# Kernel tuning notes

Hardware: AMD Instinct MI355X
Metric: run time of the kernel (lower is better)

## Reference

```python
import jax, jax.numpy as jnp
import numpy as np

DIM = 1024
NUM_HEADS = 16
REL_DIM = 32
B, N = 8, 512


def setup_inputs() -> dict:
    key = jax.random.key(0)
    ks = jax.random.split(key, 8)
    s = 0.02
    return {
        "x": jax.random.normal(ks[0], (B, N, DIM), dtype=jnp.float32),
        "rel_bias": jax.random.normal(ks[1], (B, N, N, REL_DIM), dtype=jnp.float32),
        # torch nn.Linear convention: weight (out_features, in_features)
        "W_qkv": jax.random.normal(ks[2], (3 * DIM, DIM), dtype=jnp.float32) * s,
        "b_qkv": jax.random.normal(ks[3], (3 * DIM,), dtype=jnp.float32) * s,
        "W_rel": jax.random.normal(ks[4], (NUM_HEADS, REL_DIM), dtype=jnp.float32) * s,
        "b_rel": jax.random.normal(ks[5], (NUM_HEADS,), dtype=jnp.float32) * s,
        "W_out": jax.random.normal(ks[6], (DIM, DIM), dtype=jnp.float32) * s,
        "b_out": jax.random.normal(ks[7], (DIM,), dtype=jnp.float32) * s,
    }


def reference(x, rel_bias, W_qkv, b_qkv, W_rel, b_rel, W_out, b_out):
    Bx, Nx, D = x.shape
    H = NUM_HEADS
    hd = D // H
    # QKV projection: (B,N,3D) -> (B,N,3,H,hd)
    qkv = (x @ W_qkv.T + b_qkv).reshape(Bx, Nx, 3, H, hd)
    q, k, v = qkv[:, :, 0], qkv[:, :, 1], qkv[:, :, 2]
    scale = hd ** -0.5
    attn = jnp.einsum('bnhd,bmhd->bhnm', q, k) * scale
    # per-pair relative bias projected to heads: (B,N,N,H) -> (B,H,N,N)
    rel = (rel_bias @ W_rel.T + b_rel).transpose(0, 3, 1, 2)
    attn = jax.nn.softmax(attn + rel, axis=-1)
    out = jnp.einsum('bhnm,bmhd->bnhd', attn, v).reshape(Bx, Nx, D)
    return out @ W_out.T + b_out
```

## Files before the change

kernel.cpp:

```cpp
#include <hip/hip_runtime.h>

typedef unsigned short u16;
typedef unsigned int u32;
typedef __attribute__((ext_vector_type(8))) __bf16 bf16x8;
typedef __attribute__((ext_vector_type(4))) float f32x4;

union U8 {
  bf16x8 b;
  uint2 u2[2];
  uint4 u4;
  u16 us[8];
};

__device__ __forceinline__ u16 f2bf(float f) {
  u32 x = __float_as_uint(f);
  x += 0x7FFFu + ((x >> 16) & 1u);
  return (u16)(x >> 16);
}
__device__ __forceinline__ float bf2f(u16 u) {
  return __uint_as_float(((u32)u) << 16);
}

#define GLOAD16(gp, lp)                                                          \
  __builtin_amdgcn_global_load_lds(                                              \
      (const __attribute__((address_space(1))) unsigned int*)(const void*)(gp),  \
      (__attribute__((address_space(3))) unsigned int*)(void*)(lp), 16, 0, 0)

__global__ void k_convert(const float* __restrict__ src, u16* __restrict__ dst, int n4) {
  int idx = blockIdx.x * blockDim.x + threadIdx.x;
  int stride = gridDim.x * blockDim.x;
  for (int i = idx; i < n4; i += stride) {
    float4 v = ((const float4*)src)[i];
    ushort4 o;
    o.x = f2bf(v.x); o.y = f2bf(v.y); o.z = f2bf(v.z); o.w = f2bf(v.w);
    ((ushort4*)dst)[i] = o;
  }
}

__global__ __launch_bounds__(256) void k_rel(const float* __restrict__ rb,
                                             const float* __restrict__ Wr,
                                             const float* __restrict__ br,
                                             u16* __restrict__ out) {
  __shared__ float Wl[16][32];
  __shared__ float bl[16];
  int t = threadIdx.x;
  ((float*)Wl)[t] = Wr[t];
  ((float*)Wl)[t + 256] = Wr[t + 256];
  if (t < 16) bl[t] = br[t];
  __syncthreads();

  size_t row = (size_t)blockIdx.x * 256 + t;
  int m = (int)(row & 511);
  int n = (int)((row >> 9) & 511);
  int b = (int)(row >> 18);
  const float4* rp = (const float4*)(rb + row * 32);
  float4 r4[8];
#pragma unroll
  for (int j = 0; j < 8; ++j) r4[j] = rp[j];

  size_t obase = (size_t)b * 4194304 + (size_t)n * 512 + m;
#pragma unroll
  for (int h = 0; h < 16; ++h) {
    float acc = bl[h];
    const float* w = Wl[h];
#pragma unroll
    for (int j = 0; j < 8; ++j) {
      acc += r4[j].x * w[4 * j + 0] + r4[j].y * w[4 * j + 1] +
             r4[j].z * w[4 * j + 2] + r4[j].w * w[4 * j + 3];
    }
    out[obase + (size_t)h * 262144] = f2bf(acc);
  }
}

template <int MODE>
__global__ __launch_bounds__(256) void k_gemm(const u16* __restrict__ A,
                                              const u16* __restrict__ Bm,
                                              const float* __restrict__ bias,
                                              u16* __restrict__ Qo, u16* __restrict__ Ko,
                                              u16* __restrict__ Vo, float* __restrict__ Co,
                                              int K) {
  __shared__ u16 Al[128 * 64];
  __shared__ u16 Bl[128 * 64];
  const int t = threadIdx.x;
  const int lane = t & 63, wid = t >> 6;
  const int g = lane >> 4, i16 = lane & 15;
  const int wm = wid >> 1, wn = wid & 1;
  const int bm = blockIdx.y, bn = blockIdx.x;

  f32x4 zero = {0.f, 0.f, 0.f, 0.f};
  f32x4 acc[4][4];
#pragma unroll
  for (int mi = 0; mi < 4; ++mi)
#pragma unroll
    for (int ni = 0; ni < 4; ++ni) acc[mi][ni] = zero;

  int srow[4], sgc[4];
#pragma unroll
  for (int i = 0; i < 4; ++i) {
    int ch = wid * 256 + i * 64 + lane;
    int r = ch >> 3, cs = ch & 7;
    srow[i] = r;
    sgc[i] = cs ^ (r & 7);
  }

  for (int k0 = 0; k0 < K; k0 += 64) {
    __syncthreads();
#pragma unroll
    for (int i = 0; i < 4; ++i) {
      const u16* ga = A + (size_t)(bm * 128 + srow[i]) * K + k0 + sgc[i] * 8;
      const u16* gb = Bm + (size_t)(bn * 128 + srow[i]) * K + k0 + sgc[i] * 8;
      u16* la = Al + (size_t)(wid * 256 + i * 64) * 8;
      u16* lb = Bl + (size_t)(wid * 256 + i * 64) * 8;
      GLOAD16(ga, la);
      GLOAD16(gb, lb);
    }
    __syncthreads();

#pragma unroll
    for (int kk = 0; kk < 2; ++kk) {
      U8 af[4], bfr[4];
#pragma unroll
      for (int mi = 0; mi < 4; ++mi) {
        int row = wm * 64 + mi * 16 + i16;
        int ch = (g + 4 * kk) ^ (row & 7);
        af[mi].u4 = *(const uint4*)(Al + row * 64 + ch * 8);
      }
#pragma unroll
      for (int ni = 0; ni < 4; ++ni) {
        int row = wn * 64 + ni * 16 + i16;
        int ch = (g + 4 * kk) ^ (row & 7);
        bfr[ni].u4 = *(const uint4*)(Bl + row * 64 + ch * 8);
      }
#pragma unroll
      for (int mi = 0; mi < 4; ++mi)
#pragma unroll
        for (int ni = 0; ni < 4; ++ni)
          acc[mi][ni] = __builtin_amdgcn_mfma_f32_16x16x32_bf16(af[mi].b, bfr[ni].b,
                                                                acc[mi][ni], 0, 0, 0);
    }
  }

#pragma unroll
  for (int mi = 0; mi < 4; ++mi) {
#pragma unroll
    for (int ni = 0; ni < 4; ++ni) {
      int colb = bn * 128 + wn * 64 + ni * 16;
      int col = colb + i16;
#pragma unroll
      for (int j = 0; j < 4; ++j) {
        int row = bm * 128 + wm * 64 + mi * 16 + 4 * g + j;
        float v = acc[mi][ni][j] + bias[col];
        if (MODE == 0) {
          int tt = col >> 10;
          int h = (col >> 6) & 15;
          int d = col & 63;
          int b = row >> 9;
          int n = row & 511;
          u16* dst = (tt == 0) ? Qo : ((tt == 1) ? Ko : Vo);
          dst[((size_t)(b * 16 + h) * 512 + n) * 64 + d] = f2bf(v);
        } else {
          Co[(size_t)row * 1024 + col] = v;
        }
      }
    }
  }
}

__global__ __launch_bounds__(256) void k_vt(const u16* __restrict__ V, u16* __restrict__ Vt) {
  __shared__ u16 Tl[64][72];
  const int t = threadIdx.x;
  const int n0 = blockIdx.x * 64;
  const size_t bh = blockIdx.y;
#pragma unroll
  for (int i = 0; i < 2; ++i) {
    int c = i * 256 + t;
    int r = c >> 3, c8 = (c & 7) * 8;
    U8 v;
    v.u4 = *(const uint4*)(V + (bh * 512 + n0 + r) * 64 + c8);
    *(uint2*)&Tl[r][c8] = v.u2[0];
    *(uint2*)&Tl[r][c8 + 4] = v.u2[1];
  }
  __syncthreads();
#pragma unroll
  for (int i = 0; i < 2; ++i) {
    int c = i * 256 + t;
    int d = c >> 3, n8 = (c & 7) * 8;
    U8 o;
#pragma unroll
    for (int j = 0; j < 8; ++j) o.us[j] = Tl[n8 + j][d];
    *(uint4*)(Vt + (bh * 64 + d) * 512 + n0 + n8) = o.u4;
  }
}

__global__ __launch_bounds__(256) void k_attn(const u16* __restrict__ Q,
                                              const u16* __restrict__ Kb,
                                              const u16* __restrict__ Vtb,
                                              const u16* __restrict__ Rel,
                                              u16* __restrict__ Out) {
  __shared__ u16 Kl[64 * 64];
  __shared__ u16 Vl[64 * 64];
  __shared__ u16 Pl[4][16 * 68];

  const int qt = blockIdx.x, h = blockIdx.y, b = blockIdx.z;
  const int t = threadIdx.x, lane = t & 63, wid = t >> 6;
  const int g = lane >> 4, i16 = lane & 15;
  const size_t bh = (size_t)(b * 16 + h);

  const u16* Qg = Q + (bh * 512 + qt * 64 + wid * 16 + i16) * 64;
  U8 qf[2];
  qf[0].u4 = *(const uint4*)(Qg + 8 * g);
  qf[1].u4 = *(const uint4*)(Qg + 8 * g + 32);

  float m_run[4], l_run[4];
  f32x4 zero = {0.f, 0.f, 0.f, 0.f};
  f32x4 acc[4];
#pragma unroll
  for (int c = 0; c < 4; ++c) acc[c] = zero;
#pragma unroll
  for (int j = 0; j < 4; ++j) { m_run[j] = -1e30f; l_run[j] = 0.f; }

  int srow[2], sgc[2];
#pragma unroll
  for (int i = 0; i < 2; ++i) {
    int ch = wid * 128 + i * 64 + lane;
    int r = ch >> 3, cs = ch & 7;
    srow[i] = r;
    sgc[i] = cs ^ (r & 7);
  }

  const u16* Kg0 = Kb + bh * 512 * 64;
  const u16* Vg0 = Vtb + bh * 64 * 512;
  const u16* Rg = Rel + (bh * 512 + qt * 64 + wid * 16) * 512;

  for (int m0 = 0; m0 < 512; m0 += 64) {
    __syncthreads();
#pragma unroll
    for (int i = 0; i < 2; ++i) {
      u16* lbase = (u16*)0 + (size_t)(wid * 128 + i * 64) * 8;
      GLOAD16(Kg0 + (size_t)(m0 + srow[i]) * 64 + sgc[i] * 8, Kl + (size_t)(wid * 128 + i * 64) * 8);
      GLOAD16(Vg0 + (size_t)srow[i] * 512 + m0 + sgc[i] * 8, Vl + (size_t)(wid * 128 + i * 64) * 8);
      (void)lbase;
    }
    __syncthreads();

    f32x4 s[4];
#pragma unroll
    for (int c = 0; c < 4; ++c) s[c] = zero;
#pragma unroll
    for (int c = 0; c < 4; ++c) {
#pragma unroll
      for (int kk = 0; kk < 2; ++kk) {
        int row = c * 16 + i16;
        int ch = (g + 4 * kk) ^ (row & 7);
        U8 kf;
        kf.u4 = *(const uint4*)(Kl + row * 64 + ch * 8);
        s[c] = __builtin_amdgcn_mfma_f32_16x16x32_bf16(qf[kk].b, kf.b, s[c], 0, 0, 0);
      }
    }
#pragma unroll
    for (int c = 0; c < 4; ++c) {
#pragma unroll
      for (int j = 0; j < 4; ++j) {
        float rv = bf2f(Rg[(size_t)(4 * g + j) * 512 + m0 + c * 16 + i16]);
        s[c][j] = s[c][j] * 0.125f + rv;
      }
    }
    float fac[4];
#pragma unroll
    for (int j = 0; j < 4; ++j) {
      float pm = fmaxf(fmaxf(s[0][j], s[1][j]), fmaxf(s[2][j], s[3][j]));
      pm = fmaxf(pm, __shfl_xor(pm, 1));
      pm = fmaxf(pm, __shfl_xor(pm, 2));
      pm = fmaxf(pm, __shfl_xor(pm, 4));
      pm = fmaxf(pm, __shfl_xor(pm, 8));
      float mnew = fmaxf(m_run[j], pm);
      fac[j] = __expf(m_run[j] - mnew);
      m_run[j] = mnew;
    }
#pragma unroll
    for (int c = 0; c < 4; ++c)
#pragma unroll
      for (int j = 0; j < 4; ++j) s[c][j] = __expf(s[c][j] - m_run[j]);
#pragma unroll
    for (int j = 0; j < 4; ++j) {
      float rs = s[0][j] + s[1][j] + s[2][j] + s[3][j];
      rs += __shfl_xor(rs, 1);
      rs += __shfl_xor(rs, 2);
      rs += __shfl_xor(rs, 4);
      rs += __shfl_xor(rs, 8);
      l_run[j] = l_run[j] * fac[j] + rs;
    }
#pragma unroll
    for (int c = 0; c < 4; ++c)
#pragma unroll
      for (int j = 0; j < 4; ++j) acc[c][j] *= fac[j];

    u16* Pw = Pl[wid];
#pragma unroll
    for (int c = 0; c < 4; ++c)
#pragma unroll
      for (int j = 0; j < 4; ++j)
        Pw[(4 * g + j) * 68 + c * 16 + i16] = f2bf(s[c][j]);
    __syncthreads();

    U8 pf[2];
#pragma unroll
    for (int kk = 0; kk < 2; ++kk) {
      const u16* p = Pl[wid] + i16 * 68 + 8 * g + 32 * kk;
      pf[kk].u2[0] = *(const uint2*)p;
      pf[kk].u2[1] = *(const uint2*)(p + 4);
    }
#pragma unroll
    for (int c = 0; c < 4; ++c) {
#pragma unroll
      for (int kk = 0; kk < 2; ++kk) {
        int row = c * 16 + i16;
        int ch = (g + 4 * kk) ^ (row & 7);
        U8 vf;
        vf.u4 = *(const uint4*)(Vl + row * 64 + ch * 8);
        acc[c] = __builtin_amdgcn_mfma_f32_16x16x32_bf16(pf[kk].b, vf.b, acc[c], 0, 0, 0);
      }
    }
  }

#pragma unroll
  for (int c = 0; c < 4; ++c) {
#pragma unroll
    for (int j = 0; j < 4; ++j) {
      int n = qt * 64 + wid * 16 + 4 * g + j;
      float v = acc[c][j] / l_run[j];
      Out[((size_t)b * 512 + n) * 1024 + h * 64 + c * 16 + i16] = f2bf(v);
    }
  }
}

extern "C" void kernel_launch(void* const* d_in, const int* in_sizes, int n_in,
                              void* d_out, int out_size, void* d_ws, size_t ws_size,
                              hipStream_t stream) {
  const float* x = (const float*)d_in[0];
  const float* rel_bias = (const float*)d_in[1];
  const float* W_qkv = (const float*)d_in[2];
  const float* b_qkv = (const float*)d_in[3];
  const float* W_rel = (const float*)d_in[4];
  const float* b_rel = (const float*)d_in[5];
  const float* W_out = (const float*)d_in[6];
  const float* b_out = (const float*)d_in[7];
  float* out = (float*)d_out;

  char* ws = (char*)d_ws;
  u16* x_bf    = (u16*)(ws);
  u16* Vt      = (u16*)(ws);
  u16* wqkv_bf = (u16*)(ws + 8388608);
  u16* wout_bf = (u16*)(ws + 14680064);
  u16* Qw      = (u16*)(ws + 16777216);
  u16* Kw      = (u16*)(ws + 25165824);
  u16* Vw      = (u16*)(ws + 33554432);
  u16* relb    = (u16*)(ws + 41943040);
  u16* attno   = (u16*)(ws + 109051904);

  k_convert<<<2048, 256, 0, stream>>>(x, x_bf, 4194304 / 4);
  k_convert<<<1024, 256, 0, stream>>>(W_qkv, wqkv_bf, 3145728 / 4);
  k_convert<<<512, 256, 0, stream>>>(W_out, wout_bf, 1048576 / 4);

  k_rel<<<8192, 256, 0, stream>>>(rel_bias, W_rel, b_rel, relb);

  k_gemm<0><<<dim3(24, 32), 256, 0, stream>>>(x_bf, wqkv_bf, b_qkv, Qw, Kw, Vw, nullptr, 1024);

  k_vt<<<dim3(8, 128), 256, 0, stream>>>(Vw, Vt);

  k_attn<<<dim3(8, 16, 8), 256, 0, stream>>>(Qw, Kw, Vt, relb, attno);

  k_gemm<1><<<dim3(8, 32), 256, 0, stream>>>(attno, wout_bf, b_out, nullptr, nullptr, nullptr,
                                             out, 1024);
}
```

Baseline: 200.4 us.

## Fuse conversions, tile rel-bias layout for attention, double-buffer K/V loads

Merges the three fp32-to-bf16 conversion launches into one kernel. Restructures k_rel so each thread computes four query rows and writes the projected bias in a tiled layout matching the MFMA accumulator fragments, so attention reads it with two 16-byte vector loads instead of scattered scalar loads. The attention kernel double-buffers K/V in shared memory, prefetching the next tile while computing the current one, and raises wave priority around the MFMA sections. The cost is twice the K/V shared memory and more registers in k_rel.

```diff
diff --git a/kernel.cpp b/kernel.cpp
--- a/kernel.cpp
+++ b/kernel.cpp
@@ -26,14 +26,23 @@
       (const __attribute__((address_space(1))) unsigned int*)(const void*)(gp),  \
       (__attribute__((address_space(3))) unsigned int*)(void*)(lp), 16, 0, 0)
 
-__global__ void k_convert(const float* __restrict__ src, u16* __restrict__ dst, int n4) {
+__global__ void k_convert_all(const float* __restrict__ x, const float* __restrict__ wq,
+                              const float* __restrict__ wo, u16* __restrict__ xb,
+                              u16* __restrict__ wqb, u16* __restrict__ wob) {
+  const int NX = 1048576, NQ = 786432, NO = 262144;
   int idx = blockIdx.x * blockDim.x + threadIdx.x;
   int stride = gridDim.x * blockDim.x;
-  for (int i = idx; i < n4; i += stride) {
-    float4 v = ((const float4*)src)[i];
+  for (int i = idx; i < NX + NQ + NO; i += stride) {
+    const float4* s;
+    ushort4* d;
+    int k;
+    if (i < NX) { s = (const float4*)x; d = (ushort4*)xb; k = i; }
+    else if (i < NX + NQ) { s = (const float4*)wq; d = (ushort4*)wqb; k = i - NX; }
+    else { s = (const float4*)wo; d = (ushort4*)wob; k = i - NX - NQ; }
+    float4 v = s[k];
     ushort4 o;
     o.x = f2bf(v.x); o.y = f2bf(v.y); o.z = f2bf(v.z); o.w = f2bf(v.w);
-    ((ushort4*)dst)[i] = o;
+    d[k] = o;
   }
 }
 
@@ -49,26 +58,38 @@
   if (t < 16) bl[t] = br[t];
   __syncthreads();
 
-  size_t row = (size_t)blockIdx.x * 256 + t;
-  int m = (int)(row & 511);
-  int n = (int)((row >> 9) & 511);
-  int b = (int)(row >> 18);
-  const float4* rp = (const float4*)(rb + row * 32);
-  float4 r4[8];
-#pragma unroll
-  for (int j = 0; j < 8; ++j) r4[j] = rp[j];
-
-  size_t obase = (size_t)b * 4194304 + (size_t)n * 512 + m;
+  const int c = t >> 6, lane = t & 63, g = lane >> 4, i16 = lane & 15;
+  const int mt = blockIdx.x, nt = blockIdx.y, b = blockIdx.z;
+  const int n0 = nt * 16, m0 = mt * 64;
+
+  float a[16][4];
+#pragma unroll
+  for (int j = 0; j < 4; ++j) {
+    size_t prow = ((size_t)(b * 512 + n0 + 4 * g + j)) * 512 + m0 + c * 16 + i16;
+    const float4* rp = (const float4*)(rb + prow * 32);
+    float4 r4[8];
+#pragma unroll
+    for (int q = 0; q < 8; ++q) r4[q] = rp[q];
+#pragma unroll
+    for (int h = 0; h < 16; ++h) {
+      float acc = bl[h];
+      const float* w = Wl[h];
+#pragma unroll
+      for (int q = 0; q < 8; ++q) {
+        acc += r4[q].x * w[4 * q + 0] + r4[q].y * w[4 * q + 1] +
+               r4[q].z * w[4 * q + 2] + r4[q].w * w[4 * q + 3];
+      }
+      a[h][j] = acc;
+    }
+  }
+
 #pragma unroll
   for (int h = 0; h < 16; ++h) {
-    float acc = bl[h];
-    const float* w = Wl[h];
-#pragma unroll
-    for (int j = 0; j < 8; ++j) {
-      acc += r4[j].x * w[4 * j + 0] + r4[j].y * w[4 * j + 1] +
-             r4[j].z * w[4 * j + 2] + r4[j].w * w[4 * j + 3];
-    }
-    out[obase + (size_t)h * 262144] = f2bf(acc);
+    uint2 w;
+    w.x = (u32)f2bf(a[h][0]) | ((u32)f2bf(a[h][1]) << 16);
+    w.y = (u32)f2bf(a[h][2]) | ((u32)f2bf(a[h][3]) << 16);
+    size_t o = (((size_t)(b * 16 + h) * 32 + nt) * 8 + mt) * 1024 + lane * 16 + c * 4;
+    *(uint2*)(out + o) = w;
   }
 }
 
@@ -109,10 +130,8 @@
     for (int i = 0; i < 4; ++i) {
       const u16* ga = A + (size_t)(bm * 128 + srow[i]) * K + k0 + sgc[i] * 8;
       const u16* gb = Bm + (size_t)(bn * 128 + srow[i]) * K + k0 + sgc[i] * 8;
-      u16* la = Al + (size_t)(wid * 256 + i * 64) * 8;
-      u16* lb = Bl + (size_t)(wid * 256 + i * 64) * 8;
-      GLOAD16(ga, la);
-      GLOAD16(gb, lb);
+      GLOAD16(ga, Al + (size_t)(wid * 256 + i * 64) * 8);
+      GLOAD16(gb, Bl + (size_t)(wid * 256 + i * 64) * 8);
     }
     __syncthreads();
 
@@ -197,8 +216,8 @@
                                               const u16* __restrict__ Vtb,
                                               const u16* __restrict__ Rel,
                                               u16* __restrict__ Out) {
-  __shared__ u16 Kl[64 * 64];
-  __shared__ u16 Vl[64 * 64];
+  __shared__ u16 Kl[2][64 * 64];
+  __shared__ u16 Vl[2][64 * 64];
   __shared__ u16 Pl[4][16 * 68];
 
   const int qt = blockIdx.x, h = blockIdx.y, b = blockIdx.z;
@@ -230,22 +249,34 @@
 
   const u16* Kg0 = Kb + bh * 512 * 64;
   const u16* Vg0 = Vtb + bh * 64 * 512;
-  const u16* Rg = Rel + (bh * 512 + qt * 64 + wid * 16) * 512;
-
-  for (int m0 = 0; m0 < 512; m0 += 64) {
-    __syncthreads();
-#pragma unroll
-    for (int i = 0; i < 2; ++i) {
-      u16* lbase = (u16*)0 + (size_t)(wid * 128 + i * 64) * 8;
-      GLOAD16(Kg0 + (size_t)(m0 + srow[i]) * 64 + sgc[i] * 8, Kl + (size_t)(wid * 128 + i * 64) * 8);
-      GLOAD16(Vg0 + (size_t)srow[i] * 512 + m0 + sgc[i] * 8, Vl + (size_t)(wid * 128 + i * 64) * 8);
-      (void)lbase;
-    }
-    __syncthreads();
+  const u16* Rg = Rel + ((bh * 32 + qt * 4 + wid) * 8) * 1024 + lane * 16;
+
+#define STAGE(buf, m0)                                                                  \
+  do {                                                                                  \
+    _Pragma("unroll") for (int i = 0; i < 2; ++i) {                                     \
+      GLOAD16(Kg0 + (size_t)((m0) + srow[i]) * 64 + sgc[i] * 8,                         \
+              &Kl[buf][(size_t)(wid * 128 + i * 64) * 8]);                              \
+      GLOAD16(Vg0 + (size_t)srow[i] * 512 + (m0) + sgc[i] * 8,                          \
+              &Vl[buf][(size_t)(wid * 128 + i * 64) * 8]);                              \
+    }                                                                                   \
+  } while (0)
+
+  STAGE(0, 0);
+  __syncthreads();
+
+  for (int it = 0; it < 8; ++it) {
+    const int buf = it & 1;
+    const int m0 = it * 64;
+    if (it < 7) STAGE(buf ^ 1, m0 + 64);
+
+    U8 r0_, r1_;
+    r0_.u4 = *(const uint4*)(Rg + it * 1024);
+    r1_.u4 = *(const uint4*)(Rg + it * 1024 + 8);
 
     f32x4 s[4];
 #pragma unroll
     for (int c = 0; c < 4; ++c) s[c] = zero;
+    __builtin_amdgcn_s_setprio(1);
 #pragma unroll
     for (int c = 0; c < 4; ++c) {
 #pragma unroll
@@ -253,15 +284,17 @@
         int row = c * 16 + i16;
         int ch = (g + 4 * kk) ^ (row & 7);
         U8 kf;
-        kf.u4 = *(const uint4*)(Kl + row * 64 + ch * 8);
+        kf.u4 = *(const uint4*)(&Kl[buf][row * 64 + ch * 8]);
         s[c] = __builtin_amdgcn_mfma_f32_16x16x32_bf16(qf[kk].b, kf.b, s[c], 0, 0, 0);
       }
     }
+    __builtin_amdgcn_s_setprio(0);
+
 #pragma unroll
     for (int c = 0; c < 4; ++c) {
 #pragma unroll
       for (int j = 0; j < 4; ++j) {
-        float rv = bf2f(Rg[(size_t)(4 * g + j) * 512 + m0 + c * 16 + i16]);
+        float rv = bf2f((c < 2 ? r0_ : r1_).us[(c & 1) * 4 + j]);
         s[c][j] = s[c][j] * 0.125f + rv;
       }
     }
@@ -310,6 +343,7 @@
       pf[kk].u2[0] = *(const uint2*)p;
       pf[kk].u2[1] = *(const uint2*)(p + 4);
     }
+    __builtin_amdgcn_s_setprio(1);
 #pragma unroll
     for (int c = 0; c < 4; ++c) {
 #pragma unroll
@@ -317,11 +351,14 @@
         int row = c * 16 + i16;
         int ch = (g + 4 * kk) ^ (row & 7);
         U8 vf;
-        vf.u4 = *(const uint4*)(Vl + row * 64 + ch * 8);
+        vf.u4 = *(const uint4*)(&Vl[buf][row * 64 + ch * 8]);
         acc[c] = __builtin_amdgcn_mfma_f32_16x16x32_bf16(pf[kk].b, vf.b, acc[c], 0, 0, 0);
       }
     }
-  }
+    __builtin_amdgcn_s_setprio(0);
+    __syncthreads();
+  }
+#undef STAGE
 
 #pragma unroll
   for (int c = 0; c < 4; ++c) {
@@ -358,11 +395,9 @@
   u16* relb    = (u16*)(ws + 41943040);
   u16* attno   = (u16*)(ws + 109051904);
 
-  k_convert<<<2048, 256, 0, stream>>>(x, x_bf, 4194304 / 4);
-  k_convert<<<1024, 256, 0, stream>>>(W_qkv, wqkv_bf, 3145728 / 4);
-  k_convert<<<512, 256, 0, stream>>>(W_out, wout_bf, 1048576 / 4);
-
-  k_rel<<<8192, 256, 0, stream>>>(rel_bias, W_rel, b_rel, relb);
+  k_convert_all<<<2048, 256, 0, stream>>>(x, W_qkv, W_out, x_bf, wqkv_bf, wout_bf);
+
+  k_rel<<<dim3(8, 32, 8), 256, 0, stream>>>(rel_bias, W_rel, b_rel, relb);
 
   k_gemm<0><<<dim3(24, 32), 256, 0, stream>>>(x_bf, wqkv_bf, b_qkv, Qw, Kw, Vw, nullptr, 1024);
 
```

Measured after the change: 733.0 us. 3.66x slower.
